# Kernel optimization log

Hardware: AMD Instinct MI355X
Metric: run time of the kernel (lower is better)

The kernel has to match this reference:

```python
import jax, jax.numpy as jnp
import numpy as np

N_CELLS = 16384
N_SPOTS = 4096
N_LABELS = 512
EXTENT = 1000.0  # spatial extent of the array in microns
UNDERFLOW_NU = 1e-12


def setup_inputs() -> dict:
    key = jax.random.key(0)
    k_z, k_x, k_y, k_lab = jax.random.split(key, 4)
    z = jax.random.uniform(k_z, (N_CELLS, 2), dtype=jnp.float32) * EXTENT
    encoding_x = jax.random.uniform(k_x, (N_SPOTS,), dtype=jnp.float32) * EXTENT
    encoding_y = jax.random.uniform(k_y, (N_SPOTS,), dtype=jnp.float32) * EXTENT
    spot_labels = jax.random.randint(k_lab, (N_SPOTS,), 0, N_LABELS, dtype=jnp.int32)
    diffusion_constant = jnp.float32(2500.0)  # D ~ (50 um)^2 scale so kernel is non-degenerate
    return {
        "z": z,
        "diffusion_constant": diffusion_constant,
        "encoding_x": encoding_x,
        "encoding_y": encoding_y,
        "spot_labels": spot_labels,
    }


def reference(z, diffusion_constant, encoding_x, encoding_y, spot_labels):
    # rel_distances: squared euclidean distance, (n_cells, n_spots)
    dx = encoding_x[None, :] - z[:, 0:1]
    dy = encoding_y[None, :] - z[:, 1:2]
    distances = dx * dx + dy * dy
    # diffusion_kernel (Fick's law, 2D Gaussian kernel)
    norm = 1.0 / (2.0 * jnp.pi * diffusion_constant)
    rate_per_spot = norm * jnp.exp(-distances / (2.0 * diffusion_constant)) + UNDERFLOW_NU
    # label_transfer_rate: segment-sum over spots grouped by label -> (n_cells, n_labels)
    rate_per_tag = jax.ops.segment_sum(
        rate_per_spot.T, spot_labels, num_segments=N_LABELS
    ).T
    return rate_per_tag
```

## Files before the change

kernel.cpp:

```cpp
#include <hip/hip_runtime.h>
#include <hip/hip_bf16.h>

#define N_CELLS  16384
#define N_SPOTS  4096
#define N_LABELS 512
#define NTHREADS 512
#define MTHREADS 256
#define NBUILD   8
#define CPB      8
#define NPAIR    (CPB/2)
#define TABLE    6144

typedef float v2f __attribute__((ext_vector_type(2)));
typedef float v4f __attribute__((ext_vector_type(4)));

__device__ __forceinline__ float fast_exp2(float x) {
    float r;
    asm("v_exp_f32 %0, %1" : "=v"(r) : "v"(x));
    return r;
}

#define HALF_LOG2E 0.72134752044448170f

__global__ __launch_bounds__(512) void build_kernel(
    const float* __restrict__ ex, const float* __restrict__ ey,
    const int* __restrict__ labels, const float* __restrict__ dconst,
    float2* __restrict__ table, int* __restrict__ meta)
{
    __shared__ unsigned short s_lab[N_SPOTS];
    __shared__ int s_h[NBUILD][N_LABELS];
    __shared__ int s_c[N_LABELS];
    __shared__ int s_h2[128];
    __shared__ int s_suf[128];
    __shared__ int s_pcw[32 * 8];
    __shared__ int s_rlab[N_LABELS];
    __shared__ int s_rcnt[N_LABELS];
    __shared__ int s_wmax[8];
    __shared__ int s_wbase[8];
    __shared__ int s_slot[N_LABELS];
    __shared__ int s_kcur[N_LABELS];

    const int t = threadIdx.x;
    const int lane = t & 63, w = t >> 6;
    const int b = blockIdx.x;

    #pragma unroll
    for (int q = 0; q < NBUILD; ++q) s_h[q][t] = 0;
    if (t < 128) s_h2[t] = 0;
    for (int i = t; i < N_SPOTS; i += NTHREADS) s_lab[i] = (unsigned short)labels[i];
    __syncthreads();

    for (int i = t; i < N_SPOTS; i += NTHREADS) atomicAdd(&s_h[i >> 9][s_lab[i]], 1);
    __syncthreads();

    int myc = 0, pre = 0;
    #pragma unroll
    for (int q = 0; q < NBUILD; ++q) {
        if (q == b) pre = myc;
        myc += s_h[q][t];
    }
    s_c[t] = myc;
    const int mycc = myc < 127 ? myc : 127;
    atomicAdd(&s_h2[mycc], 1);
    __syncthreads();

    if (t < 128) s_suf[t] = s_h2[t];
    __syncthreads();
    for (int off = 1; off < 128; off <<= 1) {
        int add = (t < 128 && t + off < 128) ? s_suf[t + off] : 0;
        __syncthreads();
        if (t < 128) s_suf[t] += add;
        __syncthreads();
    }

    int pos_w = 0;
    for (int v = 0; v < 32; ++v) {
        unsigned long long mask = __ballot(myc == v);
        if (myc == v) pos_w = __popcll(mask & ((1ull << lane) - 1ull));
        if (lane == 0) s_pcw[v * 8 + w] = __popcll(mask);
    }
    __syncthreads();
    int pos;
    if (myc < 32) {
        pos = pos_w;
        for (int w2 = 0; w2 < w; ++w2) pos += s_pcw[myc * 8 + w2];
    } else {
        pos = 0;
        for (int j = 0; j < t; ++j) pos += (s_c[j] == myc) ? 1 : 0;
    }
    const int r = ((myc < 127) ? s_suf[myc + 1] : 0) + pos;
    s_rlab[r] = t;
    s_rcnt[r] = myc;
    __syncthreads();

    int v = s_rcnt[t];
    #pragma unroll
    for (int off = 32; off; off >>= 1) { int o = __shfl_xor(v, off); v = v > o ? v : o; }
    if (lane == 0) s_wmax[w] = v;
    __syncthreads();
    if (t == 0) {
        int pb = 0;
        #pragma unroll
        for (int w2 = 0; w2 < 8; ++w2) { s_wbase[w2] = 64 * pb; pb += s_wmax[w2]; }
    }
    __syncthreads();

    s_slot[t] = s_wbase[r >> 6] + (r & 63);
    s_kcur[t] = pre;
    __syncthreads();

    const float Dv = dconst[0];
    const float sc = sqrtf(HALF_LOG2E / Dv);

    {
        const int i = b * NTHREADS + t;
        const int l = s_lab[i];
        const int k = atomicAdd(&s_kcur[l], 1);
        table[s_slot[l] + k * 64] = make_float2(ex[i] * sc, ey[i] * sc);
    }

    {
        const int q    = b * 64 + lane;
        const int trip = s_wmax[b];
        const int base = s_wbase[b];
        for (int k = s_rcnt[q] + (t >> 6); k < trip; k += 8)
            table[base + k * 64 + lane] = make_float2(1e8f, 0.0f);
    }

    if (b == 0) {
        meta[t]                = s_wbase[t >> 6];
        meta[NTHREADS + t]     = s_wmax[t >> 6];
        meta[2 * NTHREADS + t] = s_rlab[t];
        meta[3 * NTHREADS + t] = s_rcnt[t];
    }
}

__device__ __forceinline__ void kphase(
    const v2f* __restrict__ seg, int trip,
    const v2f* zxn, const v2f* zyn, v2f* acc)
{
    if (trip <= 0) return;
    v2f xy = seg[0];
    for (int p = 0; p < trip; ++p) {
        const int pn = (p + 1 < trip) ? p + 1 : p;
        v2f nxt = seg[(size_t)pn * 64];
        const v2f xx = (v2f){xy.x, xy.x};
        const v2f yy = (v2f){xy.y, xy.y};
        #pragma unroll
        for (int j = 0; j < NPAIR; ++j) {
            v2f dx  = xx + zxn[j];
            v2f dy  = yy + zyn[j];
            v2f m   = dy * dy;
            v2f nd2 = __builtin_elementwise_fma(-dx, dx, -m);
            v2f e   = (v2f){ fast_exp2(nd2.x), fast_exp2(nd2.y) };
            acc[j] += e;
        }
        xy = nxt;
    }
}

__global__ __launch_bounds__(256, 8) void diffusion_main_kernel(
    const float* __restrict__ z, const float* __restrict__ dconst,
    const v2f* __restrict__ table, const int* __restrict__ meta,
    float* __restrict__ out)
{
    __shared__ float tr[CPB * N_LABELS];

    const int t = threadIdx.x;
    const int lane = t & 63, w = t >> 6;

    const int p  = (w + (int)blockIdx.x) & 3;
    const int cA = p, cB = 7 - p;
    const int uA = cA * 64 + lane;
    const int uB = cB * 64 + lane;

    const int wbaseA = __builtin_amdgcn_readfirstlane(meta[uA]);
    const int tripA  = __builtin_amdgcn_readfirstlane(meta[NTHREADS + uA]);
    const int labA   = meta[2 * NTHREADS + uA];
    const float cntA = (float)meta[3 * NTHREADS + uA];
    const int wbaseB = __builtin_amdgcn_readfirstlane(meta[uB]);
    const int tripB  = __builtin_amdgcn_readfirstlane(meta[NTHREADS + uB]);
    const int labB   = meta[2 * NTHREADS + uB];
    const float cntB = (float)meta[3 * NTHREADS + uB];

    const float D    = dconst[0];
    const float sc   = sqrtf(HALF_LOG2E / D);
    const float norm = 1.0f / (6.28318530717958647f * D);
    const float baseA = cntA * 1e-12f;
    const float baseB = cntB * 1e-12f;

    const int cell0 = blockIdx.x * CPB;
    v2f zxn[NPAIR], zyn[NPAIR], accA[NPAIR], accB[NPAIR];
    #pragma unroll
    for (int j = 0; j < NPAIR; ++j) {
        zxn[j] = (v2f){ -z[2 * (cell0 + 2 * j)]     * sc,
                        -z[2 * (cell0 + 2 * j + 1)] * sc };
        zyn[j] = (v2f){ -z[2 * (cell0 + 2 * j) + 1]     * sc,
                        -z[2 * (cell0 + 2 * j + 1) + 1] * sc };
        accA[j] = (v2f){0.f, 0.f};
        accB[j] = (v2f){0.f, 0.f};
    }

    kphase(table + wbaseA + lane, tripA, zxn, zyn, accA);
    kphase(table + wbaseB + lane, tripB, zxn, zyn, accB);

    #pragma unroll
    for (int j = 0; j < NPAIR; ++j) {
        tr[(2 * j)     * N_LABELS + labA] = fmaf(accA[j].x, norm, baseA);
        tr[(2 * j + 1) * N_LABELS + labA] = fmaf(accA[j].y, norm, baseA);
        tr[(2 * j)     * N_LABELS + labB] = fmaf(accB[j].x, norm, baseB);
        tr[(2 * j + 1) * N_LABELS + labB] = fmaf(accB[j].y, norm, baseB);
    }
    __syncthreads();

    const v4f* tr4 = (const v4f*)tr;
    v4f* out4 = (v4f*)(out + (size_t)cell0 * N_LABELS);
    #pragma unroll
    for (int rr = 0; rr < CPB * N_LABELS / 4 / MTHREADS; ++rr)
        __builtin_nontemporal_store(tr4[t + rr * MTHREADS],
                                    &out4[t + rr * MTHREADS]);
}

extern "C" void kernel_launch(void* const* d_in, const int* in_sizes, int n_in,
                              void* d_out, int out_size, void* d_ws, size_t ws_size,
                              hipStream_t stream)
{
    const float* z      = (const float*)d_in[0];
    const float* dconst = (const float*)d_in[1];
    const float* ex     = (const float*)d_in[2];
    const float* ey     = (const float*)d_in[3];
    const int*   labels = (const int*)d_in[4];
    float*       out    = (float*)d_out;

    float2* table = (float2*)d_ws;
    int*    meta  = (int*)((char*)d_ws + (size_t)TABLE * sizeof(float2));

    build_kernel<<<NBUILD, NTHREADS, 0, stream>>>(ex, ey, labels, dconst, table, meta);

    diffusion_main_kernel<<<N_CELLS / CPB, MTHREADS, 0, stream>>>(
        z, dconst, (const v2f*)table, meta, out);
}
```

Baseline: 29.20 us.

## Fuse table build and main pass into one cooperative kernel with grid sync

```diff
diff --git a/kernel.cpp b/kernel.cpp
--- a/kernel.cpp
+++ b/kernel.cpp
@@ -1,13 +1,17 @@
 #include <hip/hip_runtime.h>
 #include <hip/hip_bf16.h>
+#include <hip/hip_cooperative_groups.h>
+
+namespace cg = cooperative_groups;
 
 #define N_CELLS  16384
 #define N_SPOTS  4096
 #define N_LABELS 512
-#define NTHREADS 512
 #define MTHREADS 256
+#define NBLK     1024
 #define NBUILD   8
 #define CPB      8
+#define GROUPS   2
 #define NPAIR    (CPB/2)
 #define TABLE    6144
 
@@ -22,118 +26,23 @@
 
 #define HALF_LOG2E 0.72134752044448170f
 
-__global__ __launch_bounds__(512) void build_kernel(
-    const float* __restrict__ ex, const float* __restrict__ ey,
-    const int* __restrict__ labels, const float* __restrict__ dconst,
-    float2* __restrict__ table, int* __restrict__ meta)
-{
-    __shared__ unsigned short s_lab[N_SPOTS];
-    __shared__ int s_h[NBUILD][N_LABELS];
-    __shared__ int s_c[N_LABELS];
-    __shared__ int s_h2[128];
-    __shared__ int s_suf[128];
-    __shared__ int s_pcw[32 * 8];
-    __shared__ int s_rlab[N_LABELS];
-    __shared__ int s_rcnt[N_LABELS];
-    __shared__ int s_wmax[8];
-    __shared__ int s_wbase[8];
-    __shared__ int s_slot[N_LABELS];
-    __shared__ int s_kcur[N_LABELS];
-
-    const int t = threadIdx.x;
-    const int lane = t & 63, w = t >> 6;
-    const int b = blockIdx.x;
-
-    #pragma unroll
-    for (int q = 0; q < NBUILD; ++q) s_h[q][t] = 0;
-    if (t < 128) s_h2[t] = 0;
-    for (int i = t; i < N_SPOTS; i += NTHREADS) s_lab[i] = (unsigned short)labels[i];
-    __syncthreads();
-
-    for (int i = t; i < N_SPOTS; i += NTHREADS) atomicAdd(&s_h[i >> 9][s_lab[i]], 1);
-    __syncthreads();
-
-    int myc = 0, pre = 0;
-    #pragma unroll
-    for (int q = 0; q < NBUILD; ++q) {
-        if (q == b) pre = myc;
-        myc += s_h[q][t];
-    }
-    s_c[t] = myc;
-    const int mycc = myc < 127 ? myc : 127;
-    atomicAdd(&s_h2[mycc], 1);
-    __syncthreads();
-
-    if (t < 128) s_suf[t] = s_h2[t];
-    __syncthreads();
-    for (int off = 1; off < 128; off <<= 1) {
-        int add = (t < 128 && t + off < 128) ? s_suf[t + off] : 0;
-        __syncthreads();
-        if (t < 128) s_suf[t] += add;
-        __syncthreads();
-    }
-
-    int pos_w = 0;
-    for (int v = 0; v < 32; ++v) {
-        unsigned long long mask = __ballot(myc == v);
-        if (myc == v) pos_w = __popcll(mask & ((1ull << lane) - 1ull));
-        if (lane == 0) s_pcw[v * 8 + w] = __popcll(mask);
-    }
-    __syncthreads();
-    int pos;
-    if (myc < 32) {
-        pos = pos_w;
-        for (int w2 = 0; w2 < w; ++w2) pos += s_pcw[myc * 8 + w2];
-    } else {
-        pos = 0;
-        for (int j = 0; j < t; ++j) pos += (s_c[j] == myc) ? 1 : 0;
-    }
-    const int r = ((myc < 127) ? s_suf[myc + 1] : 0) + pos;
-    s_rlab[r] = t;
-    s_rcnt[r] = myc;
-    __syncthreads();
-
-    int v = s_rcnt[t];
-    #pragma unroll
-    for (int off = 32; off; off >>= 1) { int o = __shfl_xor(v, off); v = v > o ? v : o; }
-    if (lane == 0) s_wmax[w] = v;
-    __syncthreads();
-    if (t == 0) {
-        int pb = 0;
-        #pragma unroll
-        for (int w2 = 0; w2 < 8; ++w2) { s_wbase[w2] = 64 * pb; pb += s_wmax[w2]; }
-    }
-    __syncthreads();
-
-    s_slot[t] = s_wbase[r >> 6] + (r & 63);
-    s_kcur[t] = pre;
-    __syncthreads();
-
-    const float Dv = dconst[0];
-    const float sc = sqrtf(HALF_LOG2E / Dv);
-
-    {
-        const int i = b * NTHREADS + t;
-        const int l = s_lab[i];
-        const int k = atomicAdd(&s_kcur[l], 1);
-        table[s_slot[l] + k * 64] = make_float2(ex[i] * sc, ey[i] * sc);
-    }
-
-    {
-        const int q    = b * 64 + lane;
-        const int trip = s_wmax[b];
-        const int base = s_wbase[b];
-        for (int k = s_rcnt[q] + (t >> 6); k < trip; k += 8)
-            table[base + k * 64 + lane] = make_float2(1e8f, 0.0f);
-    }
-
-    if (b == 0) {
-        meta[t]                = s_wbase[t >> 6];
-        meta[NTHREADS + t]     = s_wmax[t >> 6];
-        meta[2 * NTHREADS + t] = s_rlab[t];
-        meta[3 * NTHREADS + t] = s_rcnt[t];
-    }
-}
+union SmemU {
+    struct {
+        int pre[N_LABELS];
+        int tot[N_LABELS];
+        int h2[128];
+        int suf[128];
+        int pcwA[32 * 4];
+        int pcwB[32 * 4];
+        int rlab[N_LABELS];
+        int rcnt[N_LABELS];
+        int slot[N_LABELS];
+        int kcur[N_LABELS];
+        int wmax[8];
+        int wbase[8];
+    } b;
+    float tr[CPB * N_LABELS];
+};
 
 __device__ __forceinline__ void kphase(
     const v2f* __restrict__ seg, int trip,
@@ -159,66 +68,192 @@
     }
 }
 
-__global__ __launch_bounds__(256, 8) void diffusion_main_kernel(
+__global__ __launch_bounds__(MTHREADS, 4) void diffusion_fused_kernel(
     const float* __restrict__ z, const float* __restrict__ dconst,
-    const v2f* __restrict__ table, const int* __restrict__ meta,
+    const float* __restrict__ ex, const float* __restrict__ ey,
+    const int* __restrict__ labels,
+    float2* __restrict__ table, int* __restrict__ meta,
     float* __restrict__ out)
 {
-    __shared__ float tr[CPB * N_LABELS];
+    __shared__ SmemU smem;
 
     const int t = threadIdx.x;
     const int lane = t & 63, w = t >> 6;
-
-    const int p  = (w + (int)blockIdx.x) & 3;
+    const int bid = blockIdx.x;
+
+    if (bid < NBUILD) {
+        auto& bs = smem.b;
+        const int b = bid;
+
+        bs.pre[t] = 0; bs.pre[t + 256] = 0;
+        bs.tot[t] = 0; bs.tot[t + 256] = 0;
+        if (t < 128) bs.h2[t] = 0;
+        __syncthreads();
+
+        for (int i = t; i < 512 * b; i += MTHREADS)
+            atomicAdd(&bs.pre[labels[i]], 1);
+        __syncthreads();
+        bs.tot[t] = bs.pre[t]; bs.tot[t + 256] = bs.pre[t + 256];
+        __syncthreads();
+        for (int i = 512 * b + t; i < N_SPOTS; i += MTHREADS)
+            atomicAdd(&bs.tot[labels[i]], 1);
+        __syncthreads();
+
+        const int mycA = bs.tot[t], mycB = bs.tot[t + 256];
+        atomicAdd(&bs.h2[mycA < 127 ? mycA : 127], 1);
+        atomicAdd(&bs.h2[mycB < 127 ? mycB : 127], 1);
+        __syncthreads();
+
+        if (t < 128) bs.suf[t] = bs.h2[t];
+        __syncthreads();
+        for (int off = 1; off < 128; off <<= 1) {
+            int add = (t < 128 && t + off < 128) ? bs.suf[t + off] : 0;
+            __syncthreads();
+            if (t < 128) bs.suf[t] += add;
+            __syncthreads();
+        }
+
+        int posAw = 0, posBw = 0;
+        for (int v = 0; v < 32; ++v) {
+            unsigned long long mA = __ballot(mycA == v);
+            if (mycA == v) posAw = __popcll(mA & ((1ull << lane) - 1ull));
+            if (lane == 0) bs.pcwA[v * 4 + w] = __popcll(mA);
+            unsigned long long mB = __ballot(mycB == v);
+            if (mycB == v) posBw = __popcll(mB & ((1ull << lane) - 1ull));
+            if (lane == 0) bs.pcwB[v * 4 + w] = __popcll(mB);
+        }
+        __syncthreads();
+        int posA, posB;
+        if (mycA < 32) {
+            posA = posAw;
+            for (int w2 = 0; w2 < w; ++w2) posA += bs.pcwA[mycA * 4 + w2];
+        } else {
+            posA = 0;
+            for (int j = 0; j < t; ++j) posA += (bs.tot[j] == mycA) ? 1 : 0;
+        }
+        if (mycB < 32) {
+            posB = posBw;
+            for (int w2 = 0; w2 < 4; ++w2) posB += bs.pcwA[mycB * 4 + w2];
+            for (int w2 = 0; w2 < w; ++w2) posB += bs.pcwB[mycB * 4 + w2];
+        } else {
+            posB = 0;
+            for (int j = 0; j < t + 256; ++j) posB += (bs.tot[j] == mycB) ? 1 : 0;
+        }
+        const int rA = ((mycA < 127) ? bs.suf[mycA + 1] : 0) + posA;
+        const int rB = ((mycB < 127) ? bs.suf[mycB + 1] : 0) + posB;
+        bs.rlab[rA] = t;       bs.rcnt[rA] = mycA;
+        bs.rlab[rB] = t + 256; bs.rcnt[rB] = mycB;
+        __syncthreads();
+
+        {
+            int v0 = bs.rcnt[t], v1 = bs.rcnt[t + 256];
+            #pragma unroll
+            for (int off = 32; off; off >>= 1) {
+                int o0 = __shfl_xor(v0, off); v0 = v0 > o0 ? v0 : o0;
+                int o1 = __shfl_xor(v1, off); v1 = v1 > o1 ? v1 : o1;
+            }
+            if (lane == 0) { bs.wmax[w] = v0; bs.wmax[w + 4] = v1; }
+        }
+        __syncthreads();
+        if (t == 0) {
+            int pb = 0;
+            #pragma unroll
+            for (int c = 0; c < 8; ++c) { bs.wbase[c] = 64 * pb; pb += bs.wmax[c]; }
+        }
+        __syncthreads();
+
+        bs.slot[t]       = bs.wbase[rA >> 6] + (rA & 63);
+        bs.kcur[t]       = bs.pre[t];
+        bs.slot[t + 256] = bs.wbase[rB >> 6] + (rB & 63);
+        bs.kcur[t + 256] = bs.pre[t + 256];
+        __syncthreads();
+
+        const float Dv = dconst[0];
+        const float scb = sqrtf(HALF_LOG2E / Dv);
+
+        for (int i = 512 * b + t; i < 512 * (b + 1); i += MTHREADS) {
+            int l = labels[i];
+            int k = atomicAdd(&bs.kcur[l], 1);
+            table[bs.slot[l] + k * 64] = make_float2(ex[i] * scb, ey[i] * scb);
+        }
+        {
+            const int q    = 64 * b + (t & 63);
+            const int trip = bs.wmax[b];
+            const int base = bs.wbase[b];
+            for (int k = bs.rcnt[q] + (t >> 6); k < trip; k += 4)
+                table[base + k * 64 + (t & 63)] = make_float2(1e8f, 0.0f);
+        }
+        if (b == 0) {
+            for (int m = t; m < N_LABELS; m += MTHREADS) {
+                meta[m]        = bs.wbase[m >> 6];
+                meta[512 + m]  = bs.wmax[m >> 6];
+                meta[1024 + m] = bs.rlab[m];
+                meta[1536 + m] = bs.rcnt[m];
+            }
+        }
+        __threadfence();
+    }
+
+    cg::this_grid().sync();
+
+    const int p  = (w + bid) & 3;
     const int cA = p, cB = 7 - p;
     const int uA = cA * 64 + lane;
     const int uB = cB * 64 + lane;
 
     const int wbaseA = __builtin_amdgcn_readfirstlane(meta[uA]);
-    const int tripA  = __builtin_amdgcn_readfirstlane(meta[NTHREADS + uA]);
-    const int labA   = meta[2 * NTHREADS + uA];
-    const float cntA = (float)meta[3 * NTHREADS + uA];
+    const int tripA  = __builtin_amdgcn_readfirstlane(meta[512 + uA]);
+    const int labA   = meta[1024 + uA];
+    const float cntA = (float)meta[1536 + uA];
     const int wbaseB = __builtin_amdgcn_readfirstlane(meta[uB]);
-    const int tripB  = __builtin_amdgcn_readfirstlane(meta[NTHREADS + uB]);
-    const int labB   = meta[2 * NTHREADS + uB];
-    const float cntB = (float)meta[3 * NTHREADS + uB];
-
-    const float D    = dconst[0];
-    const float sc   = sqrtf(HALF_LOG2E / D);
-    const float norm = 1.0f / (6.28318530717958647f * D);
+    const int tripB  = __builtin_amdgcn_readfirstlane(meta[512 + uB]);
+    const int labB   = meta[1024 + uB];
+    const float cntB = (float)meta[1536 + uB];
+
+    const float D     = dconst[0];
+    const float sc    = sqrtf(HALF_LOG2E / D);
+    const float norm  = 1.0f / (6.28318530717958647f * D);
     const float baseA = cntA * 1e-12f;
     const float baseB = cntB * 1e-12f;
 
-    const int cell0 = blockIdx.x * CPB;
-    v2f zxn[NPAIR], zyn[NPAIR], accA[NPAIR], accB[NPAIR];
+    const v2f* tab = (const v2f*)table;
+    float* tr = smem.tr;
+
     #pragma unroll
-    for (int j = 0; j < NPAIR; ++j) {
-        zxn[j] = (v2f){ -z[2 * (cell0 + 2 * j)]     * sc,
-                        -z[2 * (cell0 + 2 * j + 1)] * sc };
-        zyn[j] = (v2f){ -z[2 * (cell0 + 2 * j) + 1]     * sc,
-                        -z[2 * (cell0 + 2 * j + 1) + 1] * sc };
-        accA[j] = (v2f){0.f, 0.f};
-        accB[j] = (v2f){0.f, 0.f};
+    for (int g = 0; g < GROUPS; ++g) {
+        __syncthreads();
+
+        const int cell0 = bid * (CPB * GROUPS) + g * CPB;
+        v2f zxn[NPAIR], zyn[NPAIR], accA[NPAIR], accB[NPAIR];
+        #pragma unroll
+        for (int j = 0; j < NPAIR; ++j) {
+            zxn[j] = (v2f){ -z[2 * (cell0 + 2 * j)]     * sc,
+                            -z[2 * (cell0 + 2 * j + 1)] * sc };
+            zyn[j] = (v2f){ -z[2 * (cell0 + 2 * j) + 1]     * sc,
+                            -z[2 * (cell0 + 2 * j + 1) + 1] * sc };
+            accA[j] = (v2f){0.f, 0.f};
+            accB[j] = (v2f){0.f, 0.f};
+        }
+
+        kphase(tab + wbaseA + lane, tripA, zxn, zyn, accA);
+        kphase(tab + wbaseB + lane, tripB, zxn, zyn, accB);
+
+        #pragma unroll
+        for (int j = 0; j < NPAIR; ++j) {
+            tr[(2 * j)     * N_LABELS + labA] = fmaf(accA[j].x, norm, baseA);
+            tr[(2 * j + 1) * N_LABELS + labA] = fmaf(accA[j].y, norm, baseA);
+            tr[(2 * j)     * N_LABELS + labB] = fmaf(accB[j].x, norm, baseB);
+            tr[(2 * j + 1) * N_LABELS + labB] = fmaf(accB[j].y, norm, baseB);
+        }
+        __syncthreads();
+
+        const v4f* tr4 = (const v4f*)tr;
+        v4f* out4 = (v4f*)(out + (size_t)cell0 * N_LABELS);
+        #pragma unroll
+        for (int rr = 0; rr < CPB * N_LABELS / 4 / MTHREADS; ++rr)
+            __builtin_nontemporal_store(tr4[t + rr * MTHREADS],
+                                        &out4[t + rr * MTHREADS]);
     }
-
-    kphase(table + wbaseA + lane, tripA, zxn, zyn, accA);
-    kphase(table + wbaseB + lane, tripB, zxn, zyn, accB);
-
-    #pragma unroll
-    for (int j = 0; j < NPAIR; ++j) {
-        tr[(2 * j)     * N_LABELS + labA] = fmaf(accA[j].x, norm, baseA);
-        tr[(2 * j + 1) * N_LABELS + labA] = fmaf(accA[j].y, norm, baseA);
-        tr[(2 * j)     * N_LABELS + labB] = fmaf(accB[j].x, norm, baseB);
-        tr[(2 * j + 1) * N_LABELS + labB] = fmaf(accB[j].y, norm, baseB);
-    }
-    __syncthreads();
-
-    const v4f* tr4 = (const v4f*)tr;
-    v4f* out4 = (v4f*)(out + (size_t)cell0 * N_LABELS);
-    #pragma unroll
-    for (int rr = 0; rr < CPB * N_LABELS / 4 / MTHREADS; ++rr)
-        __builtin_nontemporal_store(tr4[t + rr * MTHREADS],
-                                    &out4[t + rr * MTHREADS]);
 }
 
 extern "C" void kernel_launch(void* const* d_in, const int* in_sizes, int n_in,
@@ -235,8 +270,11 @@
     float2* table = (float2*)d_ws;
     int*    meta  = (int*)((char*)d_ws + (size_t)TABLE * sizeof(float2));
 
-    build_kernel<<<NBUILD, NTHREADS, 0, stream>>>(ex, ey, labels, dconst, table, meta);
-
-    diffusion_main_kernel<<<N_CELLS / CPB, MTHREADS, 0, stream>>>(
-        z, dconst, (const v2f*)table, meta, out);
-}
+    void* kargs[] = { (void*)&z, (void*)&dconst, (void*)&ex, (void*)&ey,
+                      (void*)&labels, (void*)&table, (void*)&meta, (void*)&out };
+
+    hipError_t err = hipLaunchCooperativeKernel(
+        (const void*)diffusion_fused_kernel,
+        dim3(NBLK), dim3(MTHREADS), kargs, 0, stream);
+    (void)err;
+}
```

New measurement: 87.00 us. 198% more time.
